# Optimization experiments

Hardware: AMD Instinct MI355X
Metric: run time of the kernel (lower is better)

Reference implementation:

```python
import jax, jax.numpy as jnp
import numpy as np


def _mlp(x, W1, b1, W2, b2):
    # Linear -> exact GELU (torch nn.GELU default) -> Linear
    h = jax.nn.gelu(x @ W1 + b1, approximate=False)
    return h @ W2 + b2


def setup_inputs() -> dict:
    B, L, H, NB, D, HID = 4, 4096, 16, 64, 1024, 128
    NS = H * NB
    key = jax.random.key(0)
    ks = jax.random.split(key, 6)
    theta_path = jax.random.normal(ks[0], (B, L, H, NB), dtype=jnp.float32)
    content_emb = jax.random.normal(ks[1], (B, L, D), dtype=jnp.float32)
    log_Pi = jnp.zeros((H, NB), dtype=jnp.float32)
    s1 = 1.0 / np.sqrt(D)
    s2 = 1.0 / np.sqrt(HID)
    # log_R_head: Linear(D,128) -> GELU -> Linear(128,NS), last weight scaled by 0.01, bias 0
    Wr1 = jax.random.uniform(ks[2], (D, HID), jnp.float32, -s1, s1)
    br1 = jnp.zeros((HID,), jnp.float32)
    Wr2 = jax.random.uniform(ks[3], (HID, NS), jnp.float32, -s2, s2) * 0.01
    br2 = jnp.zeros((NS,), jnp.float32)
    # measure_head: Linear(D,128) -> GELU -> Linear(128,NS)
    Wm1 = jax.random.uniform(ks[4], (D, HID), jnp.float32, -s1, s1)
    bm1 = jnp.zeros((HID,), jnp.float32)
    Wm2 = jax.random.uniform(ks[5], (HID, NS), jnp.float32, -s2, s2)
    bm2 = jnp.zeros((NS,), jnp.float32)
    return {
        "theta_path": theta_path, "content_emb": content_emb, "log_Pi": log_Pi,
        "Wr1": Wr1, "br1": br1, "Wr2": Wr2, "br2": br2,
        "Wm1": Wm1, "bm1": bm1, "Wm2": Wm2, "bm2": bm2,
    }


def reference(theta_path, content_emb, log_Pi, Wr1, br1, Wr2, br2, Wm1, bm1, Wm2, bm2):
    B, L, H, NB = theta_path.shape
    # per-token measurement noise R_t
    log_R = jnp.clip(_mlp(content_emb, Wr1, br1, Wr2, br2).reshape(B, L, H, NB), -5.0, 5.0)
    R = jnp.exp(log_R)
    # measurement z in (-pi, pi)
    z = jnp.pi * jnp.tanh(_mlp(content_emb, Wm1, bm1, Wm2, bm2).reshape(B, L, H, NB))
    diff = z - theta_path
    nu = jnp.arctan2(jnp.sin(diff), jnp.cos(diff))  # wrapped innovation
    Pi = jnp.exp(log_Pi)            # (H, NB) constant covariance
    Pi_b = Pi[None, None]           # (1,1,H,NB)
    K = Pi_b / jnp.maximum(Pi_b + R, 1e-8)  # Kalman gain
    alpha = 1.0 - K
    u = K * nu
    # scalar affine parallel scan: d[t] = alpha[t]*d[t-1] + u[t], d[-1]=0
    def combine(c1, c2):
        a1, v1 = c1
        a2, v2 = c2
        return a1 * a2, a2 * v1 + v2
    _, d = jax.lax.associative_scan(combine, (alpha, u), axis=1)
    theta_hat = theta_path + d
    return theta_hat, Pi, K, R
```

## Files before the change

### kernel.cpp

```cpp
#include <hip/hip_runtime.h>
#include <math.h>

static constexpr size_t OUT_THETA = 0;
static constexpr size_t OUT_PI    = 16777216;
static constexpr size_t OUT_K     = 16778240;
static constexpr size_t OUT_R     = 33555456;

#define PI_F     3.14159265358979323846f
#define INV2PI_F 0.15915494309189535f
#define PI2_HI   6.28318548202514648f
#define PI2_LO  -1.7484556e-7f
#define SPLIT_S  2048.0f
#define SPLIT_IS (1.0f / 2048.0f)

typedef _Float16 half8 __attribute__((ext_vector_type(8)));
typedef float    f32x4 __attribute__((ext_vector_type(4)));

__device__ __forceinline__ float gelu_f(float x) {
    return 0.5f * x * (1.0f + erff(x * 0.70710678118654752f));
}

__global__ __launch_bounds__(256) void k_prep(
    const float* __restrict__ Wr1, const float* __restrict__ Wm1,
    const float* __restrict__ Wr2, const float* __restrict__ Wm2,
    _Float16* __restrict__ W1rT, _Float16* __restrict__ W1mTh, _Float16* __restrict__ W1mTl,
    _Float16* __restrict__ W2rT, _Float16* __restrict__ W2mTh, _Float16* __restrict__ W2mTl)
{
    const int i = blockIdx.x * 256 + threadIdx.x;
    {
        const int k = i >> 7, c = i & 127;
        const int o = c * 1024 + k;
        W1rT[o] = (_Float16)Wr1[i];
        float w = Wm1[i];
        _Float16 h = (_Float16)w;
        W1mTh[o] = h;
        W1mTl[o] = (_Float16)((w - (float)h) * SPLIT_S);
    }
    {
        const int k = i >> 10, c = i & 1023;
        const int o = c * 128 + k;
        W2rT[o] = (_Float16)Wr2[i];
        float w = Wm2[i];
        _Float16 h = (_Float16)w;
        W2mTh[o] = h;
        W2mTl[o] = (_Float16)((w - (float)h) * SPLIT_S);
    }
}

__global__ __launch_bounds__(256, 3) void k_mm1(
    const float* __restrict__ X,
    const _Float16* __restrict__ WrT,
    const _Float16* __restrict__ WmTh, const _Float16* __restrict__ WmTl,
    const float* __restrict__ br1, const float* __restrict__ bm1,
    _Float16* __restrict__ OHr, _Float16* __restrict__ OHmh, _Float16* __restrict__ OHml)
{
    __shared__ _Float16 sm[20480];
    _Float16* XH = sm;
    _Float16* XL = sm + 2560;
    _Float16* WR = sm + 5120;
    _Float16* WH = sm + 10240;
    _Float16* WL = sm + 15360;

    const int m0   = blockIdx.x * 64;
    const int tid  = threadIdx.x;
    const int lane = tid & 63;
    const int quad = lane >> 4, l15 = lane & 15;
    const int rt   = tid >> 6;
    const int arow = tid >> 2, aseg = tid & 3;

    f32x4 accR[8] = {};
    f32x4 accA[8] = {};
    f32x4 accB[8] = {};

    for (int k0 = 0; k0 < 1024; k0 += 32) {
        const float* xp = X + (size_t)(m0 + arow) * 1024 + k0 + aseg * 8;
        float4 xa = *(const float4*)(xp);
        float4 xb = *(const float4*)(xp + 4);
        half8 wr[2], wh[2], wl[2];
#pragma unroll
        for (int it = 0; it < 2; ++it) {
            const int u = tid + it * 256;
            const int col = u >> 2, ws = u & 3;
            const size_t go = (size_t)col * 1024 + k0 + ws * 8;
            wr[it] = *(const half8*)(WrT  + go);
            wh[it] = *(const half8*)(WmTh + go);
            wl[it] = *(const half8*)(WmTl + go);
        }
        __syncthreads();
        {
            half8 hh, hl;
#pragma unroll
            for (int c = 0; c < 8; ++c) {
                float v = (c < 4) ? ((const float*)&xa)[c] : ((const float*)&xb)[c - 4];
                _Float16 h = (_Float16)v;
                hh[c] = h;
                hl[c] = (_Float16)((v - (float)h) * SPLIT_S);
            }
            *(half8*)&XH[arow * 40 + aseg * 8] = hh;
            *(half8*)&XL[arow * 40 + aseg * 8] = hl;
        }
#pragma unroll
        for (int it = 0; it < 2; ++it) {
            const int u = tid + it * 256;
            const int col = u >> 2, ws = u & 3;
            *(half8*)&WR[col * 40 + ws * 8] = wr[it];
            *(half8*)&WH[col * 40 + ws * 8] = wh[it];
            *(half8*)&WL[col * 40 + ws * 8] = wl[it];
        }
        __syncthreads();
        half8 ah = *(const half8*)&XH[(rt * 16 + l15) * 40 + quad * 8];
        half8 al = *(const half8*)&XL[(rt * 16 + l15) * 40 + quad * 8];
#pragma unroll
        for (int ct = 0; ct < 8; ++ct) {
            half8 bhr = *(const half8*)&WR[(ct * 16 + l15) * 40 + quad * 8];
            accR[ct] = __builtin_amdgcn_mfma_f32_16x16x32_f16(ah, bhr, accR[ct], 0, 0, 0);
            half8 bhm = *(const half8*)&WH[(ct * 16 + l15) * 40 + quad * 8];
            accA[ct] = __builtin_amdgcn_mfma_f32_16x16x32_f16(ah, bhm, accA[ct], 0, 0, 0);
            half8 blm = *(const half8*)&WL[(ct * 16 + l15) * 40 + quad * 8];
            accB[ct] = __builtin_amdgcn_mfma_f32_16x16x32_f16(ah, blm, accB[ct], 0, 0, 0);
            accB[ct] = __builtin_amdgcn_mfma_f32_16x16x32_f16(al, bhm, accB[ct], 0, 0, 0);
        }
    }
#pragma unroll
    for (int ct = 0; ct < 8; ++ct) {
        const int col = ct * 16 + l15;
        const float bR = br1[col];
        const float bM = bm1[col];
#pragma unroll
        for (int reg = 0; reg < 4; ++reg) {
            const int token = m0 + rt * 16 + quad * 4 + reg;
            const size_t o = (size_t)token * 128 + col;
            float gr = gelu_f(accR[ct][reg] + bR);
            OHr[o] = (_Float16)gr;
            float gm = gelu_f(accA[ct][reg] + accB[ct][reg] * SPLIT_IS + bM);
            _Float16 h = (_Float16)gm;
            OHmh[o] = h;
            OHml[o] = (_Float16)((gm - (float)h) * SPLIT_S);
        }
    }
}

__global__ __launch_bounds__(256, 4) void k_mm2(
    const _Float16* __restrict__ Hr, const _Float16* __restrict__ Hmh, const _Float16* __restrict__ Hml,
    const _Float16* __restrict__ W2rT, const _Float16* __restrict__ W2mTh, const _Float16* __restrict__ W2mTl,
    const float* __restrict__ br2, const float* __restrict__ bm2,
    const float* __restrict__ log_Pi, const float* __restrict__ theta,
    float* __restrict__ out, float* __restrict__ Aws, float* __restrict__ Uws)
{
    __shared__ _Float16 sm[15360];
    _Float16* AHr = sm;
    _Float16* AHm = sm + 2560;
    _Float16* ALm = sm + 5120;
    _Float16* BHr = sm + 7680;
    _Float16* BHm = sm + 10240;
    _Float16* BLm = sm + 12800;

    const int tt = blockIdx.x;
    const int jt = blockIdx.y;
    const int m0 = tt * 64, n0 = jt * 64;
    const int tid  = threadIdx.x;
    const int lane = tid & 63;
    const int quad = lane >> 4, l15 = lane & 15;
    const int ct   = tid >> 6;
    const int row  = tid >> 2, seg = tid & 3;

    f32x4 accr[4] = {};
    f32x4 accA[4] = {};
    f32x4 accB[4] = {};

    for (int k0 = 0; k0 < 128; k0 += 32) {
        const size_t ao = (size_t)(m0 + row) * 128 + k0 + seg * 8;
        const size_t bo = (size_t)(n0 + row) * 128 + k0 + seg * 8;
        half8 la = *(const half8*)(Hr  + ao);
        half8 lb = *(const half8*)(Hmh + ao);
        half8 lc = *(const half8*)(Hml + ao);
        half8 ld = *(const half8*)(W2rT  + bo);
        half8 le = *(const half8*)(W2mTh + bo);
        half8 lf = *(const half8*)(W2mTl + bo);
        __syncthreads();
        const int so = row * 40 + seg * 8;
        *(half8*)&AHr[so] = la;
        *(half8*)&AHm[so] = lb;
        *(half8*)&ALm[so] = lc;
        *(half8*)&BHr[so] = ld;
        *(half8*)&BHm[so] = le;
        *(half8*)&BLm[so] = lf;
        __syncthreads();
        const int bidx = (ct * 16 + l15) * 40 + quad * 8;
        half8 br_ = *(const half8*)&BHr[bidx];
        half8 bm_ = *(const half8*)&BHm[bidx];
        half8 bl_ = *(const half8*)&BLm[bidx];
#pragma unroll
        for (int rt = 0; rt < 4; ++rt) {
            const int aidx = (rt * 16 + l15) * 40 + quad * 8;
            half8 a_r = *(const half8*)&AHr[aidx];
            half8 a_h = *(const half8*)&AHm[aidx];
            half8 a_l = *(const half8*)&ALm[aidx];
            accr[rt] = __builtin_amdgcn_mfma_f32_16x16x32_f16(a_r, br_, accr[rt], 0, 0, 0);
            accA[rt] = __builtin_amdgcn_mfma_f32_16x16x32_f16(a_h, bm_, accA[rt], 0, 0, 0);
            accB[rt] = __builtin_amdgcn_mfma_f32_16x16x32_f16(a_h, bl_, accB[rt], 0, 0, 0);
            accB[rt] = __builtin_amdgcn_mfma_f32_16x16x32_f16(a_l, bm_, accB[rt], 0, 0, 0);
        }
    }

    const int col = n0 + ct * 16 + l15;
    const float Pi_  = expf(log_Pi[col]);
    const float b2rv = br2[col];
    const float b2mv = bm2[col];
    float segA[4], segU[4];
#pragma unroll
    for (int rt = 0; rt < 4; ++rt) {
        float A = 1.0f, U = 0.0f;
#pragma unroll
        for (int reg = 0; reg < 4; ++reg) {
            const int token = m0 + rt * 16 + quad * 4 + reg;
            const size_t idx = (size_t)token * 1024 + col;
            float lr = fminf(fmaxf(accr[rt][reg] + b2rv, -5.0f), 5.0f);
            float R  = expf(lr);
            float Kg = __fdividef(Pi_, fmaxf(Pi_ + R, 1e-8f));
            float zp = accA[rt][reg] + accB[rt][reg] * SPLIT_IS + b2mv;
            float z  = PI_F * tanhf(zp);
            float d  = z - theta[idx];
            float n  = rintf(d * INV2PI_F);
            float nu = fmaf(-n, PI2_HI, d);
            nu       = fmaf(-n, PI2_LO, nu);
            float u  = Kg * nu;
            float al = 1.0f - Kg;
            U = fmaf(al, U, u);
            A *= al;
            out[OUT_K + idx]     = Kg;
            out[OUT_R + idx]     = R;
            out[OUT_THETA + idx] = u;
        }
        segA[rt] = A; segU[rt] = U;
    }
    __syncthreads();
    float* cA = (float*)sm;
    float* cU = cA + 1088;
    const int colLocal = ct * 16 + l15;
#pragma unroll
    for (int rt = 0; rt < 4; ++rt) {
        cA[colLocal * 17 + rt * 4 + quad] = segA[rt];
        cU[colLocal * 17 + rt * 4 + quad] = segU[rt];
    }
    __syncthreads();
    if (tid < 64) {
        float A = 1.0f, U = 0.0f;
#pragma unroll
        for (int s = 0; s < 16; ++s) {
            float a = cA[tid * 17 + s];
            float u = cU[tid * 17 + s];
            U = fmaf(a, U, u);
            A *= a;
        }
        Aws[(size_t)tt * 1024 + n0 + tid] = A;
        Uws[(size_t)tt * 1024 + n0 + tid] = U;
    }
}

__global__ __launch_bounds__(256) void k_carry(
    const float* __restrict__ Aws, const float* __restrict__ Uws, float* __restrict__ Cws,
    const float* __restrict__ log_Pi, float* __restrict__ out)
{
    const int b = blockIdx.x >> 2;
    const int j = (blockIdx.x & 3) * 256 + threadIdx.x;
    if (blockIdx.x < 4) out[OUT_PI + j] = expf(log_Pi[j]);
    float carry = 0.0f;
    for (int c = 0; c < 64; ++c) {
        const size_t off = (size_t)(b * 64 + c) * 1024 + j;
        float a = Aws[off], u = Uws[off];
        Cws[off] = carry;
        carry = fmaf(a, carry, u);
    }
}

__global__ __launch_bounds__(256) void k_apply(
    const float* __restrict__ theta, const float* __restrict__ Cws, float* __restrict__ out)
{
    const int bid = blockIdx.x;
    const int jg = bid & 3;
    const int c  = (bid >> 2) & 63;
    const int b  = bid >> 8;
    const int j  = jg * 256 + threadIdx.x;
    float d = Cws[(size_t)(b * 64 + c) * 1024 + j];
    size_t idx = (size_t)(b * 4096 + c * 64) * 1024 + j;
    const float* __restrict__ Kbase = out + OUT_K;
#pragma unroll 4
    for (int i = 0; i < 64; ++i) {
        float Kg = Kbase[idx];
        float u  = out[idx];
        d = fmaf(1.0f - Kg, d, u);
        out[idx] = theta[idx] + d;
        idx += 1024;
    }
}

extern "C" void kernel_launch(void* const* d_in, const int* in_sizes, int n_in,
                              void* d_out, int out_size, void* d_ws, size_t ws_size,
                              hipStream_t stream)
{
    const float* theta = (const float*)d_in[0];
    const float* x     = (const float*)d_in[1];
    const float* logPi = (const float*)d_in[2];
    const float* Wr1   = (const float*)d_in[3];
    const float* br1   = (const float*)d_in[4];
    const float* Wr2   = (const float*)d_in[5];
    const float* br2   = (const float*)d_in[6];
    const float* Wm1   = (const float*)d_in[7];
    const float* bm1   = (const float*)d_in[8];
    const float* Wm2   = (const float*)d_in[9];
    const float* bm2   = (const float*)d_in[10];
    float* out = (float*)d_out;

    _Float16* Hr    = (_Float16*)d_ws;
    _Float16* Hmh   = Hr  + (size_t)16384 * 128;
    _Float16* Hml   = Hmh + (size_t)16384 * 128;
    _Float16* W1rT  = Hml + (size_t)16384 * 128;
    _Float16* W1mTh = W1rT  + 131072;
    _Float16* W1mTl = W1mTh + 131072;
    _Float16* W2rT  = W1mTl + 131072;
    _Float16* W2mTh = W2rT  + 131072;
    _Float16* W2mTl = W2mTh + 131072;
    float* Aws = (float*)(W2mTl + 131072);
    float* Uws = Aws + 262144;
    float* Cws = Uws + 262144;

    k_prep<<<512, 256, 0, stream>>>(Wr1, Wm1, Wr2, Wm2,
                                    W1rT, W1mTh, W1mTl, W2rT, W2mTh, W2mTl);
    k_mm1<<<256, 256, 0, stream>>>(x, W1rT, W1mTh, W1mTl, br1, bm1, Hr, Hmh, Hml);
    k_mm2<<<dim3(256, 16), 256, 0, stream>>>(Hr, Hmh, Hml, W2rT, W2mTh, W2mTl,
                                             br2, bm2, logPi, theta, out, Aws, Uws);
    k_carry<<<16, 256, 0, stream>>>(Aws, Uws, Cws, logPi, out);
    k_apply<<<1024, 256, 0, stream>>>(theta, Cws, out);
}
```

Before: 474.6 us.

## Register-prefetch next K tile in GEMMs and vectorize carry/apply scan kernels

```diff
diff --git a/kernel.cpp b/kernel.cpp
--- a/kernel.cpp
+++ b/kernel.cpp
@@ -54,51 +54,38 @@
     const float* __restrict__ br1, const float* __restrict__ bm1,
     _Float16* __restrict__ OHr, _Float16* __restrict__ OHmh, _Float16* __restrict__ OHml)
 {
-    __shared__ _Float16 sm[20480];
-    _Float16* XH = sm;
-    _Float16* XL = sm + 2560;
-    _Float16* WR = sm + 5120;
-    _Float16* WH = sm + 10240;
-    _Float16* WL = sm + 15360;
+    __shared__ _Float16 sm[15360];
+    _Float16* WR = sm;
+    _Float16* WH = sm + 5120;
+    _Float16* WL = sm + 10240;
 
     const int m0   = blockIdx.x * 64;
     const int tid  = threadIdx.x;
     const int lane = tid & 63;
     const int quad = lane >> 4, l15 = lane & 15;
     const int rt   = tid >> 6;
-    const int arow = tid >> 2, aseg = tid & 3;
 
     f32x4 accR[8] = {};
     f32x4 accA[8] = {};
     f32x4 accB[8] = {};
 
+    const float* xp = X + (size_t)(m0 + rt * 16 + l15) * 1024 + quad * 8;
+    float4 xa = *(const float4*)(xp);
+    float4 xb = *(const float4*)(xp + 4);
+
+    half8 wr[2], wh[2], wl[2];
+#pragma unroll
+    for (int it = 0; it < 2; ++it) {
+        const int u = tid + it * 256;
+        const int col = u >> 2, ws = u & 3;
+        const size_t go = (size_t)col * 1024 + ws * 8;
+        wr[it] = *(const half8*)(WrT  + go);
+        wh[it] = *(const half8*)(WmTh + go);
+        wl[it] = *(const half8*)(WmTl + go);
+    }
+
     for (int k0 = 0; k0 < 1024; k0 += 32) {
-        const float* xp = X + (size_t)(m0 + arow) * 1024 + k0 + aseg * 8;
-        float4 xa = *(const float4*)(xp);
-        float4 xb = *(const float4*)(xp + 4);
-        half8 wr[2], wh[2], wl[2];
-#pragma unroll
-        for (int it = 0; it < 2; ++it) {
-            const int u = tid + it * 256;
-            const int col = u >> 2, ws = u & 3;
-            const size_t go = (size_t)col * 1024 + k0 + ws * 8;
-            wr[it] = *(const half8*)(WrT  + go);
-            wh[it] = *(const half8*)(WmTh + go);
-            wl[it] = *(const half8*)(WmTl + go);
-        }
         __syncthreads();
-        {
-            half8 hh, hl;
-#pragma unroll
-            for (int c = 0; c < 8; ++c) {
-                float v = (c < 4) ? ((const float*)&xa)[c] : ((const float*)&xb)[c - 4];
-                _Float16 h = (_Float16)v;
-                hh[c] = h;
-                hl[c] = (_Float16)((v - (float)h) * SPLIT_S);
-            }
-            *(half8*)&XH[arow * 40 + aseg * 8] = hh;
-            *(half8*)&XL[arow * 40 + aseg * 8] = hl;
-        }
 #pragma unroll
         for (int it = 0; it < 2; ++it) {
             const int u = tid + it * 256;
@@ -108,8 +95,27 @@
             *(half8*)&WL[col * 40 + ws * 8] = wl[it];
         }
         __syncthreads();
-        half8 ah = *(const half8*)&XH[(rt * 16 + l15) * 40 + quad * 8];
-        half8 al = *(const half8*)&XL[(rt * 16 + l15) * 40 + quad * 8];
+        half8 ah, al;
+#pragma unroll
+        for (int c = 0; c < 8; ++c) {
+            float v = (c < 4) ? ((const float*)&xa)[c] : ((const float*)&xb)[c - 4];
+            _Float16 h = (_Float16)v;
+            ah[c] = h;
+            al[c] = (_Float16)((v - (float)h) * SPLIT_S);
+        }
+        if (k0 + 32 < 1024) {
+            xa = *(const float4*)(xp + k0 + 32);
+            xb = *(const float4*)(xp + k0 + 36);
+#pragma unroll
+            for (int it = 0; it < 2; ++it) {
+                const int u = tid + it * 256;
+                const int col = u >> 2, ws = u & 3;
+                const size_t go = (size_t)col * 1024 + k0 + 32 + ws * 8;
+                wr[it] = *(const half8*)(WrT  + go);
+                wh[it] = *(const half8*)(WmTh + go);
+                wl[it] = *(const half8*)(WmTl + go);
+            }
+        }
 #pragma unroll
         for (int ct = 0; ct < 8; ++ct) {
             half8 bhr = *(const half8*)&WR[(ct * 16 + l15) * 40 + quad * 8];
@@ -168,15 +174,16 @@
     f32x4 accA[4] = {};
     f32x4 accB[4] = {};
 
+    const size_t aobase = (size_t)(m0 + row) * 128 + seg * 8;
+    const size_t bobase = (size_t)(n0 + row) * 128 + seg * 8;
+    half8 la = *(const half8*)(Hr    + aobase);
+    half8 lb = *(const half8*)(Hmh   + aobase);
+    half8 lc = *(const half8*)(Hml   + aobase);
+    half8 ld = *(const half8*)(W2rT  + bobase);
+    half8 le = *(const half8*)(W2mTh + bobase);
+    half8 lf = *(const half8*)(W2mTl + bobase);
+
     for (int k0 = 0; k0 < 128; k0 += 32) {
-        const size_t ao = (size_t)(m0 + row) * 128 + k0 + seg * 8;
-        const size_t bo = (size_t)(n0 + row) * 128 + k0 + seg * 8;
-        half8 la = *(const half8*)(Hr  + ao);
-        half8 lb = *(const half8*)(Hmh + ao);
-        half8 lc = *(const half8*)(Hml + ao);
-        half8 ld = *(const half8*)(W2rT  + bo);
-        half8 le = *(const half8*)(W2mTh + bo);
-        half8 lf = *(const half8*)(W2mTl + bo);
         __syncthreads();
         const int so = row * 40 + seg * 8;
         *(half8*)&AHr[so] = la;
@@ -186,6 +193,14 @@
         *(half8*)&BHm[so] = le;
         *(half8*)&BLm[so] = lf;
         __syncthreads();
+        if (k0 + 32 < 128) {
+            la = *(const half8*)(Hr    + aobase + k0 + 32);
+            lb = *(const half8*)(Hmh   + aobase + k0 + 32);
+            lc = *(const half8*)(Hml   + aobase + k0 + 32);
+            ld = *(const half8*)(W2rT  + bobase + k0 + 32);
+            le = *(const half8*)(W2mTh + bobase + k0 + 32);
+            lf = *(const half8*)(W2mTl + bobase + k0 + 32);
+        }
         const int bidx = (ct * 16 + l15) * 40 + quad * 8;
         half8 br_ = *(const half8*)&BHr[bidx];
         half8 bm_ = *(const half8*)&BHm[bidx];
@@ -262,15 +277,25 @@
     const float* __restrict__ Aws, const float* __restrict__ Uws, float* __restrict__ Cws,
     const float* __restrict__ log_Pi, float* __restrict__ out)
 {
-    const int b = blockIdx.x >> 2;
-    const int j = (blockIdx.x & 3) * 256 + threadIdx.x;
-    if (blockIdx.x < 4) out[OUT_PI + j] = expf(log_Pi[j]);
-    float carry = 0.0f;
+    const int b  = blockIdx.x;
+    const int j4 = threadIdx.x;
+    if (b == 0) {
+        float4 lp = *(const float4*)(log_Pi + j4 * 4);
+        float4 p;
+        p.x = expf(lp.x); p.y = expf(lp.y); p.z = expf(lp.z); p.w = expf(lp.w);
+        *(float4*)(out + OUT_PI + j4 * 4) = p;
+    }
+    float4 carry = {0.0f, 0.0f, 0.0f, 0.0f};
+#pragma unroll 8
     for (int c = 0; c < 64; ++c) {
-        const size_t off = (size_t)(b * 64 + c) * 1024 + j;
-        float a = Aws[off], u = Uws[off];
-        Cws[off] = carry;
-        carry = fmaf(a, carry, u);
+        const size_t off = (size_t)(b * 64 + c) * 1024 + j4 * 4;
+        float4 a = *(const float4*)(Aws + off);
+        float4 u = *(const float4*)(Uws + off);
+        *(float4*)(Cws + off) = carry;
+        carry.x = fmaf(a.x, carry.x, u.x);
+        carry.y = fmaf(a.y, carry.y, u.y);
+        carry.z = fmaf(a.z, carry.z, u.z);
+        carry.w = fmaf(a.w, carry.w, u.w);
     }
 }
 
@@ -278,19 +303,24 @@
     const float* __restrict__ theta, const float* __restrict__ Cws, float* __restrict__ out)
 {
     const int bid = blockIdx.x;
-    const int jg = bid & 3;
-    const int c  = (bid >> 2) & 63;
-    const int b  = bid >> 8;
-    const int j  = jg * 256 + threadIdx.x;
-    float d = Cws[(size_t)(b * 64 + c) * 1024 + j];
-    size_t idx = (size_t)(b * 4096 + c * 64) * 1024 + j;
+    const int c   = bid & 63;
+    const int b   = bid >> 6;
+    const int j0  = threadIdx.x * 4;
+    float4 d = *(const float4*)(Cws + (size_t)(b * 64 + c) * 1024 + j0);
+    size_t idx = (size_t)(b * 4096 + c * 64) * 1024 + j0;
     const float* __restrict__ Kbase = out + OUT_K;
 #pragma unroll 4
     for (int i = 0; i < 64; ++i) {
-        float Kg = Kbase[idx];
-        float u  = out[idx];
-        d = fmaf(1.0f - Kg, d, u);
-        out[idx] = theta[idx] + d;
+        float4 Kg = *(const float4*)(Kbase + idx);
+        float4 u  = *(const float4*)(out + idx);
+        float4 th = *(const float4*)(theta + idx);
+        d.x = fmaf(1.0f - Kg.x, d.x, u.x);
+        d.y = fmaf(1.0f - Kg.y, d.y, u.y);
+        d.z = fmaf(1.0f - Kg.z, d.z, u.z);
+        d.w = fmaf(1.0f - Kg.w, d.w, u.w);
+        float4 r;
+        r.x = th.x + d.x; r.y = th.y + d.y; r.z = th.z + d.z; r.w = th.w + d.w;
+        *(float4*)(out + idx) = r;
         idx += 1024;
     }
 }
@@ -330,6 +360,6 @@
     k_mm1<<<256, 256, 0, stream>>>(x, W1rT, W1mTh, W1mTl, br1, bm1, Hr, Hmh, Hml);
     k_mm2<<<dim3(256, 16), 256, 0, stream>>>(Hr, Hmh, Hml, W2rT, W2mTh, W2mTl,
                                              br2, bm2, logPi, theta, out, Aws, Uws);
-    k_carry<<<16, 256, 0, stream>>>(Aws, Uws, Cws, logPi, out);
-    k_apply<<<1024, 256, 0, stream>>>(theta, Cws, out);
-}
+    k_carry<<<4, 256, 0, stream>>>(Aws, Uws, Cws, logPi, out);
+    k_apply<<<256, 256, 0, stream>>>(theta, Cws, out);
+}
```

Measured after the change: 470.1 us. No clear change (-1.0%).
